# Performance work log

Measured on AMD Instinct MI355X. Metric: run time of the kernel, lower is better.

The kernel has to match this reference:

```python
import jax, jax.numpy as jnp
import numpy as np

EPS = 1e-5  # nn.LayerNorm default eps
N_LAYERS, N, D_IN, H, D_OUT, NH = 4, 2048, 512, 1024, 256, 16


def setup_inputs() -> dict:
    key = jax.random.key(0)
    ks = jax.random.split(key, 8)
    s = lambda k, shape: (jax.random.normal(k, shape, jnp.float32) * 0.02)
    return {
        "x": jax.random.normal(ks[0], (N, D_IN), jnp.float32),
        "W1": s(ks[1], (H, D_IN)), "b1": jnp.zeros((H,), jnp.float32),
        # per-layer MHA params, stacked on a leading layer axis
        "Wqkv": s(ks[2], (N_LAYERS, 3 * H, H)), "bqkv": jnp.zeros((N_LAYERS, 3 * H), jnp.float32),
        "Wo": s(ks[3], (N_LAYERS, H, H)), "bo": jnp.zeros((N_LAYERS, H), jnp.float32),
        "ln_g": jnp.ones((N_LAYERS, H), jnp.float32), "ln_b": jnp.zeros((N_LAYERS, H), jnp.float32),
        "W2": s(ks[4], (D_OUT, H)), "b2": jnp.zeros((D_OUT,), jnp.float32),
        "g_out": jnp.ones((D_OUT,), jnp.float32), "b_out": jnp.zeros((D_OUT,), jnp.float32),
        "num_heads": NH,
    }


def layer_norm(x, g, b):
    m = jnp.mean(x, axis=-1, keepdims=True)
    v = jnp.mean(jnp.square(x - m), axis=-1, keepdims=True)
    return (x - m) * jax.lax.rsqrt(v + EPS) * g + b


def mha(x, Wqkv, bqkv, Wo, bo, nh):
    # x: [N, H]; attention is over the N axis (torch MHA with batch_first=False, batch=1)
    n, h = x.shape
    hd = h // nh
    qkv = x @ Wqkv.T + bqkv                      # [N, 3H]
    q, k, v = jnp.split(qkv, 3, axis=-1)
    q = q.reshape(n, nh, hd).transpose(1, 0, 2)  # [nh, N, hd]
    k = k.reshape(n, nh, hd).transpose(1, 0, 2)
    v = v.reshape(n, nh, hd).transpose(1, 0, 2)
    scale = jnp.float32(1.0 / np.sqrt(hd))
    scores = jnp.einsum('hnd,hmd->hnm', q, k) * scale  # [nh, N, N]
    attn = jax.nn.softmax(scores, axis=-1)
    out = jnp.einsum('hnm,hmd->hnd', attn, v)          # [nh, N, hd]
    out = out.transpose(1, 0, 2).reshape(n, h)
    return out @ Wo.T + bo


def reference(x, W1, b1, Wqkv, bqkv, Wo, bo, ln_g, ln_b, W2, b2, g_out, b_out, num_heads):
    h = jax.nn.relu(x @ W1.T + b1)  # dropout is identity in eval mode
    for i in range(Wqkv.shape[0]):
        a = mha(h, Wqkv[i], bqkv[i], Wo[i], bo[i], num_heads)
        h = layer_norm(a + h, ln_g[i], ln_b[i])
    y = jax.nn.relu(h @ W2.T + b2)
    return layer_norm(y, g_out, b_out)
```

## Files before the change

kernel.cpp:

```cpp
#include <hip/hip_runtime.h>

typedef __attribute__((ext_vector_type(8))) short short8;
typedef __attribute__((ext_vector_type(4))) float f32x4;
typedef __attribute__((ext_vector_type(16))) float f32x16;
typedef __attribute__((ext_vector_type(4))) float float4v;
typedef __attribute__((ext_vector_type(4))) unsigned short ushort4v;
typedef __attribute__((ext_vector_type(4))) unsigned int uint4v;
typedef __attribute__((ext_vector_type(2))) unsigned int uint2v;

#define MFMA16(a, b, c) __builtin_amdgcn_mfma_f32_16x16x32_bf16((a), (b), (c), 0, 0, 0)
#define MFMA32(a, b, c) __builtin_amdgcn_mfma_f32_32x32x16_bf16((a), (b), (c), 0, 0, 0)
#define GLOAD_LDS16(g, s)                                                         \
  __builtin_amdgcn_global_load_lds((const __attribute__((address_space(1))) void*)(g), \
                                   (__attribute__((address_space(3))) void*)(s), 16, 0, 0)
#define EXP2(x) __builtin_amdgcn_exp2f(x)

__device__ __forceinline__ unsigned short f2bf(float f) {
  unsigned u = __builtin_bit_cast(unsigned, f);
  u += 0x7fffu + ((u >> 16) & 1u);
  return (unsigned short)(u >> 16);
}

__device__ __forceinline__ unsigned cvtpk(float lo, float hi) {
  unsigned r;
  asm("v_cvt_pk_bf16_f32 %0, %1, %2" : "=v"(r) : "v"(lo), "v"(hi));
  return r;
}

__device__ __forceinline__ void swap32(unsigned& a, unsigned& b) {
  asm volatile("v_permlane32_swap_b32 %0, %1" : "+v"(a), "+v"(b));
}

__device__ __forceinline__ float bflo(unsigned u) {
  return __builtin_bit_cast(float, u << 16);
}
__device__ __forceinline__ float bfhi(unsigned u) {
  return __builtin_bit_cast(float, u & 0xffff0000u);
}
__device__ __forceinline__ float bf2f(unsigned short u) {
  return __builtin_bit_cast(float, (unsigned)u << 16);
}

struct CvtArgs {
  const float* s[5];
  unsigned short* d[5];
  int off[6];
};

__global__ __launch_bounds__(256) void cvt_multi(CvtArgs a, int ntot4) {
  int i4 = blockIdx.x * 256 + threadIdx.x;
  const int stride = gridDim.x * 256;
  for (; i4 < ntot4; i4 += stride) {
    const int idx = i4 * 4;
    int s = 0;
#pragma unroll
    for (int k = 0; k < 4; ++k) s += (idx >= a.off[k + 1]) ? 1 : 0;
    const int local = idx - a.off[s];
    float4v v = *(const float4v*)(a.s[s] + local);
    ushort4v o;
    o.x = f2bf(v.x); o.y = f2bf(v.y); o.z = f2bf(v.z); o.w = f2bf(v.w);
    *(ushort4v*)(a.d[s] + local) = o;
  }
}

template <int BM, int BN, bool RELU, bool RES, bool OUTF, bool OUTB, bool OUTT>
__global__ __launch_bounds__(256) void gemm_bt(const unsigned short* __restrict__ A,
                                               const unsigned short* __restrict__ B,
                                               const float* __restrict__ bias,
                                               const unsigned short* __restrict__ resB,
                                               float* __restrict__ outF,
                                               unsigned short* __restrict__ outB,
                                               unsigned short* __restrict__ outT,
                                               int tcol0, int ldt,
                                               int M, int N, int K) {
  __shared__ __align__(16) unsigned short As[2][BM * 32];
  __shared__ __align__(16) unsigned short Bs[2][BN * 32];
  constexpr int MI = BM / 32, MJ = BN / 32, CA = BM / 64, CB = BN / 64;
  const int tid = threadIdx.x;
  const int w = tid >> 6, lane = tid & 63;
  const int l15 = lane & 15, l4 = lane >> 4;

  const int nwg = gridDim.x;
  const int wg = (blockIdx.x & 7) * (nwg >> 3) + (blockIdx.x >> 3);
  const int nbx = N / BN;
  const int rowBase = (wg / nbx) * BM;
  const int colBase = (wg % nbx) * BN;
  const int wm = w >> 1, wn = w & 1;

  f32x4 acc[MI][MJ] = {};

  auto stage = [&](int buf, int k0) {
#pragma unroll
    for (int i = 0; i < CA; ++i) {
      const int c = i * 256 + tid;
      GLOAD_LDS16(A + (size_t)(rowBase + (c >> 2)) * K + k0 + ((c & 3) << 3),
                  As[buf] + i * 2048 + w * 512);
    }
#pragma unroll
    for (int i = 0; i < CB; ++i) {
      const int c = i * 256 + tid;
      GLOAD_LDS16(B + (size_t)(colBase + (c >> 2)) * K + k0 + ((c & 3) << 3),
                  Bs[buf] + i * 2048 + w * 512);
    }
  };

  stage(0, 0);
  __syncthreads();

  int p = 0;
  for (int k0 = 0; k0 < K; k0 += 32) {
    if (k0 + 32 < K) stage(p ^ 1, k0 + 32);

    short8 af[MI], bf[MJ];
#pragma unroll
    for (int f = 0; f < MI; ++f)
      af[f] = *(const short8*)(As[p] + (wm * (BM / 2) + f * 16 + l15) * 32 + l4 * 8);
#pragma unroll
    for (int f = 0; f < MJ; ++f)
      bf[f] = *(const short8*)(Bs[p] + (wn * (BN / 2) + f * 16 + l15) * 32 + l4 * 8);
#pragma unroll
    for (int i = 0; i < MI; ++i)
#pragma unroll
      for (int j = 0; j < MJ; ++j)
        acc[i][j] = MFMA16(af[i], bf[j], acc[i][j]);

    __syncthreads();
    p ^= 1;
  }

#pragma unroll
  for (int i = 0; i < MI; ++i) {
    const int row0 = rowBase + wm * (BM / 2) + i * 16 + l4 * 4;
#pragma unroll
    for (int j = 0; j < MJ; ++j) {
      const int col = colBase + wn * (BN / 2) + j * 16 + l15;
      const float bv = bias[col];
      float vv[4];
#pragma unroll
      for (int e = 0; e < 4; ++e) {
        float v = acc[i][j][e] + bv;
        if constexpr (RELU) v = fmaxf(v, 0.f);
        if constexpr (RES) v += bf2f(resB[(size_t)(row0 + e) * N + col]);
        vv[e] = v;
        if constexpr (OUTF) outF[(size_t)(row0 + e) * N + col] = v;
        if constexpr (OUTB) outB[(size_t)(row0 + e) * N + col] = f2bf(v);
      }
      if constexpr (OUTT) {
        if (col >= tcol0) {
          ushort4v t;
          t.x = f2bf(vv[0]); t.y = f2bf(vv[1]); t.z = f2bf(vv[2]); t.w = f2bf(vv[3]);
          *(ushort4v*)(outT + (size_t)(col - tcol0) * ldt + row0) = t;
        }
      }
    }
  }
}

__global__ __launch_bounds__(256, 4) void flash_attn4(const unsigned short* __restrict__ qkv,
                                                      const unsigned short* __restrict__ vt,
                                                      unsigned short* __restrict__ Op0,
                                                      unsigned short* __restrict__ OpR,
                                                      float* __restrict__ Ml,
                                                      float* __restrict__ Ll,
                                                      int Nseq) {
  __shared__ __align__(16) unsigned short Ks[2][64 * 64];
  __shared__ __align__(16) unsigned short Vs[2][64 * 64];
  const int tid = threadIdx.x, w = tid >> 6, lane = tid & 63;
  const int l31 = lane & 31, l2h = lane >> 5, l7 = l31 & 7;
  const float CSC = 0.18033688011112042f;

  const int b = blockIdx.x;
  const int head = (b & 7) * 2 + ((b >> 3) & 1);
  const int s = (b >> 4) & 3;
  const int qb = b >> 6;
  const int q0w = qb * 128 + w * 32;

  const unsigned short* Qp = qkv + head * 64;
  const unsigned short* Kp = qkv + 1024 + head * 64;
  const unsigned short* Vtp = vt + (size_t)head * 64 * Nseq;

  short8 qf[4];
#pragma unroll
  for (int ka = 0; ka < 4; ++ka)
    qf[ka] = *(const short8*)(Qp + (size_t)(q0w + l31) * 3072 + ka * 16 + l2h * 8);

  f32x16 OT0 = {}, OT1 = {};
  float m = -1e30f, ls = 0.f;

  const int sr = tid >> 3, su = tid & 7;
  const int sOffA = sr * 64 + ((su ^ (sr & 7)) * 8);
  const int sOffB = sOffA + 32 * 64;

  const int kt0 = s * (Nseq >> 2);
  const int NIT = Nseq >> 8;

  short8 k0 = *(const short8*)(Kp + (size_t)(kt0 + sr) * 3072 + su * 8);
  short8 k1 = *(const short8*)(Kp + (size_t)(kt0 + sr + 32) * 3072 + su * 8);
  short8 v0 = *(const short8*)(Vtp + (size_t)sr * Nseq + kt0 + su * 8);
  short8 v1 = *(const short8*)(Vtp + (size_t)(sr + 32) * Nseq + kt0 + su * 8);
  *(short8*)(Ks[0] + sOffA) = k0;
  *(short8*)(Ks[0] + sOffB) = k1;
  *(short8*)(Vs[0] + sOffA) = v0;
  *(short8*)(Vs[0] + sOffB) = v1;
  __syncthreads();

  int p = 0;
  for (int it = 0; it < NIT; ++it) {
    const bool more = (it + 1) < NIT;
    if (more) {
      const int ktn = kt0 + (it + 1) * 64;
      k0 = *(const short8*)(Kp + (size_t)(ktn + sr) * 3072 + su * 8);
      k1 = *(const short8*)(Kp + (size_t)(ktn + sr + 32) * 3072 + su * 8);
      v0 = *(const short8*)(Vtp + (size_t)sr * Nseq + ktn + su * 8);
      v1 = *(const short8*)(Vtp + (size_t)(sr + 32) * Nseq + ktn + su * 8);
    }
    const unsigned short* KS = Ks[p];
    const unsigned short* VS = Vs[p];

    f32x16 S0 = {}, S1 = {};
    __builtin_amdgcn_s_setprio(1);
#pragma unroll
    for (int ka = 0; ka < 4; ++ka) {
      const int un = ((ka * 2 + l2h) ^ l7) * 8;
      const short8 a0 = *(const short8*)(KS + l31 * 64 + un);
      const short8 a1 = *(const short8*)(KS + (32 + l31) * 64 + un);
      S0 = MFMA32(a0, qf[ka], S0);
      S1 = MFMA32(a1, qf[ka], S1);
    }
    __builtin_amdgcn_s_setprio(0);

    float pm = S0[0];
#pragma unroll
    for (int r = 1; r < 16; ++r) pm = fmaxf(pm, S0[r]);
#pragma unroll
    for (int r = 0; r < 16; ++r) pm = fmaxf(pm, S1[r]);
    pm = fmaxf(pm, __shfl_xor(pm, 32));
    pm *= CSC;

    if (__any(pm > m + 8.f)) {
      const float mn = fmaxf(m, pm);
      const float fac = EXP2(m - mn);
      m = mn;
      ls *= fac;
#pragma unroll
      for (int r = 0; r < 16; ++r) { OT0[r] *= fac; OT1[r] *= fac; }
    }

    float rs = 0.f;
    unsigned W0[4][2], W1[4][2];
#pragma unroll
    for (int g = 0; g < 4; ++g) {
      const float a0 = EXP2(fmaf(S0[4 * g + 0], CSC, -m));
      const float a1 = EXP2(fmaf(S0[4 * g + 1], CSC, -m));
      const float a2 = EXP2(fmaf(S0[4 * g + 2], CSC, -m));
      const float a3 = EXP2(fmaf(S0[4 * g + 3], CSC, -m));
      const float b0 = EXP2(fmaf(S1[4 * g + 0], CSC, -m));
      const float b1 = EXP2(fmaf(S1[4 * g + 1], CSC, -m));
      const float b2 = EXP2(fmaf(S1[4 * g + 2], CSC, -m));
      const float b3 = EXP2(fmaf(S1[4 * g + 3], CSC, -m));
      rs += ((a0 + a1) + (a2 + a3)) + ((b0 + b1) + (b2 + b3));
      W0[g][0] = cvtpk(a0, a1); W0[g][1] = cvtpk(a2, a3);
      W1[g][0] = cvtpk(b0, b1); W1[g][1] = cvtpk(b2, b3);
    }
    rs += __shfl_xor(rs, 32);
    ls += rs;

    short8 pf[2][2];
#pragma unroll
    for (int ka = 0; ka < 2; ++ka) {
      {
        unsigned x0 = W0[2 * ka][0], y0 = W0[2 * ka + 1][0];
        unsigned x1 = W0[2 * ka][1], y1 = W0[2 * ka + 1][1];
        swap32(x0, y0);
        swap32(x1, y1);
        uint4v u = {x0, x1, y0, y1};
        pf[0][ka] = __builtin_bit_cast(short8, u);
      }
      {
        unsigned x0 = W1[2 * ka][0], y0 = W1[2 * ka + 1][0];
        unsigned x1 = W1[2 * ka][1], y1 = W1[2 * ka + 1][1];
        swap32(x0, y0);
        swap32(x1, y1);
        uint4v u = {x0, x1, y0, y1};
        pf[1][ka] = __builtin_bit_cast(short8, u);
      }
    }

    __builtin_amdgcn_s_setprio(1);
#pragma unroll
    for (int sub = 0; sub < 2; ++sub)
#pragma unroll
      for (int ka = 0; ka < 2; ++ka) {
        const int un = ((sub * 4 + ka * 2 + l2h) ^ l7) * 8;
        const short8 va0 = *(const short8*)(VS + l31 * 64 + un);
        const short8 va1 = *(const short8*)(VS + (32 + l31) * 64 + un);
        OT0 = MFMA32(va0, pf[sub][ka], OT0);
        OT1 = MFMA32(va1, pf[sub][ka], OT1);
      }
    __builtin_amdgcn_s_setprio(0);

    if (more) {
      unsigned short* Kn = Ks[p ^ 1];
      unsigned short* Vn = Vs[p ^ 1];
      *(short8*)(Kn + sOffA) = k0;
      *(short8*)(Kn + sOffB) = k1;
      *(short8*)(Vn + sOffA) = v0;
      *(short8*)(Vn + sOffB) = v1;
    }
    __syncthreads();
    p ^= 1;
  }

  unsigned short* Ob = (s == 0) ? Op0 : (OpR + (size_t)(s - 1) * Nseq * 1024);
  const int q = q0w + l31;
#pragma unroll
  for (int g = 0; g < 4; ++g) {
    const int d0 = 8 * g + 4 * l2h;
    uint2v t0 = {cvtpk(OT0[4 * g], OT0[4 * g + 1]), cvtpk(OT0[4 * g + 2], OT0[4 * g + 3])};
    uint2v t1 = {cvtpk(OT1[4 * g], OT1[4 * g + 1]), cvtpk(OT1[4 * g + 2], OT1[4 * g + 3])};
    *(uint2v*)(Ob + (size_t)q * 1024 + head * 64 + d0) = t0;
    *(uint2v*)(Ob + (size_t)q * 1024 + head * 64 + 32 + d0) = t1;
  }
  if (l2h == 0) {
    Ml[(size_t)(s * 16 + head) * Nseq + q] = m;
    Ll[(size_t)(s * 16 + head) * Nseq + q] = ls;
  }
}

__global__ __launch_bounds__(256) void attn_combine4(const unsigned short* __restrict__ Op0,
                                                     const unsigned short* __restrict__ OpR,
                                                     const float* __restrict__ Ml,
                                                     const float* __restrict__ Ll,
                                                     unsigned short* __restrict__ out, int Nseq) {
  const int t = blockIdx.x * 256 + threadIdx.x;
  const int q = t >> 8, c4 = (t & 255) * 4;
  const int head = c4 >> 6;
  float mm[4], lv[4];
  float M = -1e30f;
#pragma unroll
  for (int s = 0; s < 4; ++s) {
    mm[s] = Ml[(size_t)(s * 16 + head) * Nseq + q];
    lv[s] = Ll[(size_t)(s * 16 + head) * Nseq + q];
    M = fmaxf(M, mm[s]);
  }
  float denom = 0.f;
  float4v acc = {0.f, 0.f, 0.f, 0.f};
#pragma unroll
  for (int s = 0; s < 4; ++s) {
    const float ww = EXP2(mm[s] - M);
    denom += lv[s] * ww;
    const unsigned short* Ob = (s == 0) ? Op0 : (OpR + (size_t)(s - 1) * Nseq * 1024);
    uint2v o = *(const uint2v*)(Ob + (size_t)q * 1024 + c4);
    acc.x += bflo(o.x) * ww;
    acc.y += bfhi(o.x) * ww;
    acc.z += bflo(o.y) * ww;
    acc.w += bfhi(o.y) * ww;
  }
  const float inv = 1.f / denom;
  ushort4v r;
  r.x = f2bf(acc.x * inv);
  r.y = f2bf(acc.y * inv);
  r.z = f2bf(acc.z * inv);
  r.w = f2bf(acc.w * inv);
  *(ushort4v*)(out + (size_t)q * 1024 + c4) = r;
}

template <int D, bool WF, bool WB>
__global__ __launch_bounds__(256) void ln_rows(const float* __restrict__ src,
                                               const float* __restrict__ gw,
                                               const float* __restrict__ bw,
                                               float* __restrict__ outF,
                                               unsigned short* __restrict__ outB) {
  __shared__ float red[4];
  const int row = blockIdx.x;
  const int tid = threadIdx.x, w = tid >> 6;
  constexpr int PT = D / 256;
  const float* r = src + (size_t)row * D;
  float v[PT];
  float s = 0.f;
#pragma unroll
  for (int i = 0; i < PT; ++i) { v[i] = r[tid + i * 256]; s += v[i]; }
#pragma unroll
  for (int off = 32; off; off >>= 1) s += __shfl_down(s, off);
  if ((tid & 63) == 0) red[w] = s;
  __syncthreads();
  const float mean = (red[0] + red[1] + red[2] + red[3]) / D;
  __syncthreads();
  float q = 0.f;
#pragma unroll
  for (int i = 0; i < PT; ++i) { const float d = v[i] - mean; q += d * d; }
#pragma unroll
  for (int off = 32; off; off >>= 1) q += __shfl_down(q, off);
  if ((tid & 63) == 0) red[w] = q;
  __syncthreads();
  const float rstd = rsqrtf((red[0] + red[1] + red[2] + red[3]) / D + 1e-5f);
#pragma unroll
  for (int i = 0; i < PT; ++i) {
    const int c = tid + i * 256;
    const float o = (v[i] - mean) * rstd * gw[c] + bw[c];
    if constexpr (WF) outF[(size_t)row * D + c] = o;
    if constexpr (WB) outB[(size_t)row * D + c] = f2bf(o);
  }
}

extern "C" void kernel_launch(void* const* d_in, const int* in_sizes, int n_in,
                              void* d_out, int out_size, void* d_ws, size_t ws_size,
                              hipStream_t stream) {
  const int N = 2048, D_IN = 512, H = 1024, D_OUT = 256, NL = 4;
  const float* x    = (const float*)d_in[0];
  const float* W1   = (const float*)d_in[1];
  const float* b1   = (const float*)d_in[2];
  const float* Wqkv = (const float*)d_in[3];
  const float* bqkv = (const float*)d_in[4];
  const float* Wo   = (const float*)d_in[5];
  const float* bo   = (const float*)d_in[6];
  const float* lng  = (const float*)d_in[7];
  const float* lnb  = (const float*)d_in[8];
  const float* W2   = (const float*)d_in[9];
  const float* b2   = (const float*)d_in[10];
  const float* gout = (const float*)d_in[11];
  const float* bout = (const float*)d_in[12];
  float* out = (float*)d_out;

  char* ws = (char*)d_ws;
  auto alloc = [&](size_t bytes) -> char* {
    char* p = ws;
    ws += (bytes + 255) & ~(size_t)255;
    return p;
  };
  unsigned short* xb    = (unsigned short*)alloc((size_t)N * D_IN * 2);
  unsigned short* W1b   = (unsigned short*)alloc((size_t)H * D_IN * 2);
  unsigned short* Wqkvb = (unsigned short*)alloc((size_t)NL * 3 * H * H * 2);
  unsigned short* Wob   = (unsigned short*)alloc((size_t)NL * H * H * 2);
  unsigned short* W2b   = (unsigned short*)alloc((size_t)D_OUT * H * 2);
  unsigned short* hb    = (unsigned short*)alloc((size_t)N * H * 2);
  unsigned short* qkvb  = (unsigned short*)alloc((size_t)N * 3 * H * 2);
  unsigned short* aob   = (unsigned short*)alloc((size_t)N * H * 2);
  unsigned short* vtg   = (unsigned short*)alloc((size_t)H * N * 2);
  unsigned short* opb0  = (unsigned short*)alloc((size_t)N * H * 2);
  unsigned short* opbR  = (unsigned short*)alloc((size_t)3 * N * H * 2);
  float* af  = (float*)alloc((size_t)N * H * 4);
  float* ml  = (float*)alloc((size_t)4 * 16 * N * 4);
  float* ll  = (float*)alloc((size_t)4 * 16 * N * 4);
  float* yf  = (float*)alloc((size_t)N * D_OUT * 4);

  CvtArgs ca;
  ca.s[0] = x;    ca.d[0] = xb;
  ca.s[1] = W1;   ca.d[1] = W1b;
  ca.s[2] = Wqkv; ca.d[2] = Wqkvb;
  ca.s[3] = Wo;   ca.d[3] = Wob;
  ca.s[4] = W2;   ca.d[4] = W2b;
  const int n0 = N * D_IN, n1 = H * D_IN, n2 = NL * 3 * H * H, n3 = NL * H * H, n4 = D_OUT * H;
  ca.off[0] = 0;
  ca.off[1] = n0;
  ca.off[2] = n0 + n1;
  ca.off[3] = n0 + n1 + n2;
  ca.off[4] = n0 + n1 + n2 + n3;
  ca.off[5] = n0 + n1 + n2 + n3 + n4;
  const int ntot4 = ca.off[5] / 4;
  cvt_multi<<<2048, 256, 0, stream>>>(ca, ntot4);

  gemm_bt<64, 64, true, false, false, true, false><<<(N / 64) * (H / 64), 256, 0, stream>>>(
      xb, W1b, b1, nullptr, nullptr, hb, nullptr, 0, 0, N, H, D_IN);

  for (int l = 0; l < NL; ++l) {
    gemm_bt<128, 128, false, false, false, true, true><<<(N / 128) * (3 * H / 128), 256, 0, stream>>>(
        hb, Wqkvb + (size_t)l * 3 * H * H, bqkv + (size_t)l * 3 * H, nullptr, nullptr, qkvb,
        vtg, 2 * H, N, N, 3 * H, H);
    flash_attn4<<<1024, 256, 0, stream>>>(qkvb, vtg, opb0, opbR, ml, ll, N);
    attn_combine4<<<(N * H / 4) / 256, 256, 0, stream>>>(opb0, opbR, ml, ll, aob, N);
    gemm_bt<64, 64, false, true, true, false, false><<<(N / 64) * (H / 64), 256, 0, stream>>>(
        aob, Wob + (size_t)l * H * H, bo + (size_t)l * H, hb, af, nullptr, nullptr, 0, 0,
        N, H, H);
    ln_rows<1024, false, true><<<N, 256, 0, stream>>>(af, lng + (size_t)l * H,
                                                      lnb + (size_t)l * H, nullptr, hb);
  }

  gemm_bt<64, 64, true, false, true, false, false><<<(N / 64) * (D_OUT / 64), 256, 0, stream>>>(
      hb, W2b, b2, nullptr, yf, nullptr, nullptr, 0, 0, N, D_OUT, H);
  ln_rows<256, true, false><<<N, 256, 0, stream>>>(yf, gout, bout, out, nullptr);
}
```

Baseline: 378.0 us.

## Fuse fp32-to-bf16 weight conversion into GEMM loads and vectorize combine and layernorm

Removes the standalone conversion kernel. GEMMs now read fp32 inputs and weights through registers, convert them with packed bf16 instructions and write them to LDS inside the software pipeline. This drops a full pass over about 70MB of weights, but each GEMM now reads fp32 weights (twice the bytes) and loses the async global-to-LDS path on the B operand. The change also widens attn_combine to 8 elements per thread, vectorizes layernorm with float4, and skips writing the V columns to the row-major qkv buffer.

```diff
diff --git a/kernel.cpp b/kernel.cpp
--- a/kernel.cpp
+++ b/kernel.cpp
@@ -41,31 +41,10 @@
   return __builtin_bit_cast(float, (unsigned)u << 16);
 }
 
-struct CvtArgs {
-  const float* s[5];
-  unsigned short* d[5];
-  int off[6];
-};
-
-__global__ __launch_bounds__(256) void cvt_multi(CvtArgs a, int ntot4) {
-  int i4 = blockIdx.x * 256 + threadIdx.x;
-  const int stride = gridDim.x * 256;
-  for (; i4 < ntot4; i4 += stride) {
-    const int idx = i4 * 4;
-    int s = 0;
-#pragma unroll
-    for (int k = 0; k < 4; ++k) s += (idx >= a.off[k + 1]) ? 1 : 0;
-    const int local = idx - a.off[s];
-    float4v v = *(const float4v*)(a.s[s] + local);
-    ushort4v o;
-    o.x = f2bf(v.x); o.y = f2bf(v.y); o.z = f2bf(v.z); o.w = f2bf(v.w);
-    *(ushort4v*)(a.d[s] + local) = o;
-  }
-}
-
-template <int BM, int BN, bool RELU, bool RES, bool OUTF, bool OUTB, bool OUTT>
-__global__ __launch_bounds__(256) void gemm_bt(const unsigned short* __restrict__ A,
-                                               const unsigned short* __restrict__ B,
+template <int BM, int BN, bool AF32, bool BF32, bool RELU, bool RES,
+          bool OUTF, bool OUTB, bool OUTT>
+__global__ __launch_bounds__(256) void gemm_bt(const void* __restrict__ Av,
+                                               const void* __restrict__ Bv,
                                                const float* __restrict__ bias,
                                                const unsigned short* __restrict__ resB,
                                                float* __restrict__ outF,
@@ -73,6 +52,10 @@
                                                unsigned short* __restrict__ outT,
                                                int tcol0, int ldt,
                                                int M, int N, int K) {
+  const unsigned short* Ab = (const unsigned short*)Av;
+  const float* Af = (const float*)Av;
+  const unsigned short* Bb = (const unsigned short*)Bv;
+  const float* Bf = (const float*)Bv;
   __shared__ __align__(16) unsigned short As[2][BM * 32];
   __shared__ __align__(16) unsigned short Bs[2][BN * 32];
   constexpr int MI = BM / 32, MJ = BN / 32, CA = BM / 64, CB = BN / 64;
@@ -88,28 +71,72 @@
   const int wm = w >> 1, wn = w & 1;
 
   f32x4 acc[MI][MJ] = {};
-
-  auto stage = [&](int buf, int k0) {
+  float fA[CA][8], fB[CB][8];
+
+  auto issueA = [&](int buf, int k0) {
 #pragma unroll
     for (int i = 0; i < CA; ++i) {
       const int c = i * 256 + tid;
-      GLOAD_LDS16(A + (size_t)(rowBase + (c >> 2)) * K + k0 + ((c & 3) << 3),
-                  As[buf] + i * 2048 + w * 512);
-    }
+      if constexpr (AF32) {
+        const float* src = Af + (size_t)(rowBase + (c >> 2)) * K + k0 + ((c & 3) << 3);
+        *(float4v*)(&fA[i][0]) = *(const float4v*)src;
+        *(float4v*)(&fA[i][4]) = *(const float4v*)(src + 4);
+      } else {
+        GLOAD_LDS16(Ab + (size_t)(rowBase + (c >> 2)) * K + k0 + ((c & 3) << 3),
+                    As[buf] + i * 2048 + w * 512);
+      }
+    }
+  };
+  auto issueB = [&](int buf, int k0) {
 #pragma unroll
     for (int i = 0; i < CB; ++i) {
       const int c = i * 256 + tid;
-      GLOAD_LDS16(B + (size_t)(colBase + (c >> 2)) * K + k0 + ((c & 3) << 3),
-                  Bs[buf] + i * 2048 + w * 512);
+      if constexpr (BF32) {
+        const float* src = Bf + (size_t)(colBase + (c >> 2)) * K + k0 + ((c & 3) << 3);
+        *(float4v*)(&fB[i][0]) = *(const float4v*)src;
+        *(float4v*)(&fB[i][4]) = *(const float4v*)(src + 4);
+      } else {
+        GLOAD_LDS16(Bb + (size_t)(colBase + (c >> 2)) * K + k0 + ((c & 3) << 3),
+                    Bs[buf] + i * 2048 + w * 512);
+      }
     }
   };
-
-  stage(0, 0);
+  auto writeA = [&](int buf) {
+    if constexpr (AF32) {
+#pragma unroll
+      for (int i = 0; i < CA; ++i) {
+        const int c = i * 256 + tid;
+        uint4v u = {cvtpk(fA[i][0], fA[i][1]), cvtpk(fA[i][2], fA[i][3]),
+                    cvtpk(fA[i][4], fA[i][5]), cvtpk(fA[i][6], fA[i][7])};
+        *(uint4v*)(As[buf] + (size_t)c * 8) = u;
+      }
+    }
+  };
+  auto writeB = [&](int buf) {
+    if constexpr (BF32) {
+#pragma unroll
+      for (int i = 0; i < CB; ++i) {
+        const int c = i * 256 + tid;
+        uint4v u = {cvtpk(fB[i][0], fB[i][1]), cvtpk(fB[i][2], fB[i][3]),
+                    cvtpk(fB[i][4], fB[i][5]), cvtpk(fB[i][6], fB[i][7])};
+        *(uint4v*)(Bs[buf] + (size_t)c * 8) = u;
+      }
+    }
+  };
+
+  issueA(0, 0);
+  issueB(0, 0);
+  writeA(0);
+  writeB(0);
   __syncthreads();
 
   int p = 0;
   for (int k0 = 0; k0 < K; k0 += 32) {
-    if (k0 + 32 < K) stage(p ^ 1, k0 + 32);
+    const bool more = k0 + 32 < K;
+    if (more) {
+      issueA(p ^ 1, k0 + 32);
+      issueB(p ^ 1, k0 + 32);
+    }
 
     short8 af[MI], bf[MJ];
 #pragma unroll
@@ -124,6 +151,10 @@
       for (int j = 0; j < MJ; ++j)
         acc[i][j] = MFMA16(af[i], bf[j], acc[i][j]);
 
+    if (more) {
+      writeA(p ^ 1);
+      writeB(p ^ 1);
+    }
     __syncthreads();
     p ^= 1;
   }
@@ -143,7 +174,9 @@
         if constexpr (RES) v += bf2f(resB[(size_t)(row0 + e) * N + col]);
         vv[e] = v;
         if constexpr (OUTF) outF[(size_t)(row0 + e) * N + col] = v;
-        if constexpr (OUTB) outB[(size_t)(row0 + e) * N + col] = f2bf(v);
+        if constexpr (OUTB) {
+          if (!OUTT || col < tcol0) outB[(size_t)(row0 + e) * N + col] = f2bf(v);
+        }
       }
       if constexpr (OUTT) {
         if (col >= tcol0) {
@@ -333,8 +366,8 @@
                                                      const float* __restrict__ Ll,
                                                      unsigned short* __restrict__ out, int Nseq) {
   const int t = blockIdx.x * 256 + threadIdx.x;
-  const int q = t >> 8, c4 = (t & 255) * 4;
-  const int head = c4 >> 6;
+  const int q = t >> 7, c8 = (t & 127) * 8;
+  const int head = c8 >> 6;
   float mm[4], lv[4];
   float M = -1e30f;
 #pragma unroll
@@ -344,25 +377,25 @@
     M = fmaxf(M, mm[s]);
   }
   float denom = 0.f;
-  float4v acc = {0.f, 0.f, 0.f, 0.f};
+  float acc[8] = {};
 #pragma unroll
   for (int s = 0; s < 4; ++s) {
     const float ww = EXP2(mm[s] - M);
     denom += lv[s] * ww;
     const unsigned short* Ob = (s == 0) ? Op0 : (OpR + (size_t)(s - 1) * Nseq * 1024);
-    uint2v o = *(const uint2v*)(Ob + (size_t)q * 1024 + c4);
-    acc.x += bflo(o.x) * ww;
-    acc.y += bfhi(o.x) * ww;
-    acc.z += bflo(o.y) * ww;
-    acc.w += bfhi(o.y) * ww;
+    uint4v o = *(const uint4v*)(Ob + (size_t)q * 1024 + c8);
+    acc[0] += bflo(o.x) * ww; acc[1] += bfhi(o.x) * ww;
+    acc[2] += bflo(o.y) * ww; acc[3] += bfhi(o.y) * ww;
+    acc[4] += bflo(o.z) * ww; acc[5] += bfhi(o.z) * ww;
+    acc[6] += bflo(o.w) * ww; acc[7] += bfhi(o.w) * ww;
   }
   const float inv = 1.f / denom;
-  ushort4v r;
-  r.x = f2bf(acc.x * inv);
-  r.y = f2bf(acc.y * inv);
-  r.z = f2bf(acc.z * inv);
-  r.w = f2bf(acc.w * inv);
-  *(ushort4v*)(out + (size_t)q * 1024 + c4) = r;
+  uint4v r;
+  r.x = cvtpk(acc[0] * inv, acc[1] * inv);
+  r.y = cvtpk(acc[2] * inv, acc[3] * inv);
+  r.z = cvtpk(acc[4] * inv, acc[5] * inv);
+  r.w = cvtpk(acc[6] * inv, acc[7] * inv);
+  *(uint4v*)(out + (size_t)q * 1024 + c8) = r;
 }
 
 template <int D, bool WF, bool WB>
@@ -374,32 +407,54 @@
   __shared__ float red[4];
   const int row = blockIdx.x;
   const int tid = threadIdx.x, w = tid >> 6;
-  constexpr int PT = D / 256;
   const float* r = src + (size_t)row * D;
-  float v[PT];
-  float s = 0.f;
-#pragma unroll
-  for (int i = 0; i < PT; ++i) { v[i] = r[tid + i * 256]; s += v[i]; }
-#pragma unroll
-  for (int off = 32; off; off >>= 1) s += __shfl_down(s, off);
-  if ((tid & 63) == 0) red[w] = s;
-  __syncthreads();
-  const float mean = (red[0] + red[1] + red[2] + red[3]) / D;
-  __syncthreads();
-  float q = 0.f;
-#pragma unroll
-  for (int i = 0; i < PT; ++i) { const float d = v[i] - mean; q += d * d; }
-#pragma unroll
-  for (int off = 32; off; off >>= 1) q += __shfl_down(q, off);
-  if ((tid & 63) == 0) red[w] = q;
-  __syncthreads();
-  const float rstd = rsqrtf((red[0] + red[1] + red[2] + red[3]) / D + 1e-5f);
-#pragma unroll
-  for (int i = 0; i < PT; ++i) {
-    const int c = tid + i * 256;
-    const float o = (v[i] - mean) * rstd * gw[c] + bw[c];
-    if constexpr (WF) outF[(size_t)row * D + c] = o;
-    if constexpr (WB) outB[(size_t)row * D + c] = f2bf(o);
+  if constexpr (D == 1024) {
+    float4v v = ((const float4v*)r)[tid];
+    float s = (v.x + v.y) + (v.z + v.w);
+#pragma unroll
+    for (int off = 32; off; off >>= 1) s += __shfl_down(s, off);
+    if ((tid & 63) == 0) red[w] = s;
+    __syncthreads();
+    const float mean = (red[0] + red[1] + red[2] + red[3]) / D;
+    __syncthreads();
+    const float dx = v.x - mean, dy = v.y - mean, dz = v.z - mean, dw = v.w - mean;
+    float q = (dx * dx + dy * dy) + (dz * dz + dw * dw);
+#pragma unroll
+    for (int off = 32; off; off >>= 1) q += __shfl_down(q, off);
+    if ((tid & 63) == 0) red[w] = q;
+    __syncthreads();
+    const float rstd = rsqrtf((red[0] + red[1] + red[2] + red[3]) / D + 1e-5f);
+    float4v g4 = ((const float4v*)gw)[tid];
+    float4v b4 = ((const float4v*)bw)[tid];
+    float4v o;
+    o.x = dx * rstd * g4.x + b4.x;
+    o.y = dy * rstd * g4.y + b4.y;
+    o.z = dz * rstd * g4.z + b4.z;
+    o.w = dw * rstd * g4.w + b4.w;
+    if constexpr (WF) ((float4v*)(outF + (size_t)row * D))[tid] = o;
+    if constexpr (WB) {
+      uint2v u = {cvtpk(o.x, o.y), cvtpk(o.z, o.w)};
+      *(uint2v*)(outB + (size_t)row * D + tid * 4) = u;
+    }
+  } else {
+    float v = r[tid];
+    float s = v;
+#pragma unroll
+    for (int off = 32; off; off >>= 1) s += __shfl_down(s, off);
+    if ((tid & 63) == 0) red[w] = s;
+    __syncthreads();
+    const float mean = (red[0] + red[1] + red[2] + red[3]) / D;
+    __syncthreads();
+    const float d = v - mean;
+    float q = d * d;
+#pragma unroll
+    for (int off = 32; off; off >>= 1) q += __shfl_down(q, off);
+    if ((tid & 63) == 0) red[w] = q;
+    __syncthreads();
+    const float rstd = rsqrtf((red[0] + red[1] + red[2] + red[3]) / D + 1e-5f);
+    const float o = d * rstd * gw[tid] + bw[tid];
+    if constexpr (WF) outF[(size_t)row * D + tid] = o;
+    if constexpr (WB) outB[(size_t)row * D + tid] = f2bf(o);
   }
 }
 
@@ -428,11 +483,6 @@
     ws += (bytes + 255) & ~(size_t)255;
     return p;
   };
-  unsigned short* xb    = (unsigned short*)alloc((size_t)N * D_IN * 2);
-  unsigned short* W1b   = (unsigned short*)alloc((size_t)H * D_IN * 2);
-  unsigned short* Wqkvb = (unsigned short*)alloc((size_t)NL * 3 * H * H * 2);
-  unsigned short* Wob   = (unsigned short*)alloc((size_t)NL * H * H * 2);
-  unsigned short* W2b   = (unsigned short*)alloc((size_t)D_OUT * H * 2);
   unsigned short* hb    = (unsigned short*)alloc((size_t)N * H * 2);
   unsigned short* qkvb  = (unsigned short*)alloc((size_t)N * 3 * H * 2);
   unsigned short* aob   = (unsigned short*)alloc((size_t)N * H * 2);
@@ -444,39 +494,27 @@
   float* ll  = (float*)alloc((size_t)4 * 16 * N * 4);
   float* yf  = (float*)alloc((size_t)N * D_OUT * 4);
 
-  CvtArgs ca;
-  ca.s[0] = x;    ca.d[0] = xb;
-  ca.s[1] = W1;   ca.d[1] = W1b;
-  ca.s[2] = Wqkv; ca.d[2] = Wqkvb;
-  ca.s[3] = Wo;   ca.d[3] = Wob;
-  ca.s[4] = W2;   ca.d[4] = W2b;
-  const int n0 = N * D_IN, n1 = H * D_IN, n2 = NL * 3 * H * H, n3 = NL * H * H, n4 = D_OUT * H;
-  ca.off[0] = 0;
-  ca.off[1] = n0;
-  ca.off[2] = n0 + n1;
-  ca.off[3] = n0 + n1 + n2;
-  ca.off[4] = n0 + n1 + n2 + n3;
-  ca.off[5] = n0 + n1 + n2 + n3 + n4;
-  const int ntot4 = ca.off[5] / 4;
-  cvt_multi<<<2048, 256, 0, stream>>>(ca, ntot4);
-
-  gemm_bt<64, 64, true, false, false, true, false><<<(N / 64) * (H / 64), 256, 0, stream>>>(
-      xb, W1b, b1, nullptr, nullptr, hb, nullptr, 0, 0, N, H, D_IN);
+  gemm_bt<64, 64, true, true, true, false, false, true, false>
+      <<<(N / 64) * (H / 64), 256, 0, stream>>>(
+      x, W1, b1, nullptr, nullptr, hb, nullptr, 0, 0, N, H, D_IN);
 
   for (int l = 0; l < NL; ++l) {
-    gemm_bt<128, 128, false, false, false, true, true><<<(N / 128) * (3 * H / 128), 256, 0, stream>>>(
-        hb, Wqkvb + (size_t)l * 3 * H * H, bqkv + (size_t)l * 3 * H, nullptr, nullptr, qkvb,
+    gemm_bt<128, 128, false, true, false, false, false, true, true>
+        <<<(N / 128) * (3 * H / 128), 256, 0, stream>>>(
+        hb, Wqkv + (size_t)l * 3 * H * H, bqkv + (size_t)l * 3 * H, nullptr, nullptr, qkvb,
         vtg, 2 * H, N, N, 3 * H, H);
     flash_attn4<<<1024, 256, 0, stream>>>(qkvb, vtg, opb0, opbR, ml, ll, N);
-    attn_combine4<<<(N * H / 4) / 256, 256, 0, stream>>>(opb0, opbR, ml, ll, aob, N);
-    gemm_bt<64, 64, false, true, true, false, false><<<(N / 64) * (H / 64), 256, 0, stream>>>(
-        aob, Wob + (size_t)l * H * H, bo + (size_t)l * H, hb, af, nullptr, nullptr, 0, 0,
+    attn_combine4<<<1024, 256, 0, stream>>>(opb0, opbR, ml, ll, aob, N);
+    gemm_bt<64, 64, false, true, false, true, true, false, false>
+        <<<(N / 64) * (H / 64), 256, 0, stream>>>(
+        aob, Wo + (size_t)l * H * H, bo + (size_t)l * H, hb, af, nullptr, nullptr, 0, 0,
         N, H, H);
     ln_rows<1024, false, true><<<N, 256, 0, stream>>>(af, lng + (size_t)l * H,
                                                       lnb + (size_t)l * H, nullptr, hb);
   }
 
-  gemm_bt<64, 64, true, false, true, false, false><<<(N / 64) * (D_OUT / 64), 256, 0, stream>>>(
-      hb, W2b, b2, nullptr, yf, nullptr, nullptr, 0, 0, N, D_OUT, H);
+  gemm_bt<64, 64, false, true, true, false, true, false, false>
+      <<<(N / 64) * (D_OUT / 64), 256, 0, stream>>>(
+      hb, W2, b2, nullptr, yf, nullptr, nullptr, 0, 0, N, D_OUT, H);
   ln_rows<256, true, false><<<N, 256, 0, stream>>>(yf, gout, bout, out, nullptr);
 }
```

Result: slower. 419.7 us (+11.0%).
